# Kernel optimization log

Hardware: AMD Instinct MI355X
Metric: run time of the kernel (lower is better)

## Reference

```python
import jax, jax.numpy as jnp
import numpy as np

BINS = 128

def setup_inputs() -> dict:
    key = jax.random.key(0)
    k1, k2 = jax.random.split(key)
    B, S, F = 32, 16384, 64
    x = jax.random.uniform(k1, (B, S, F), dtype=jnp.float32)  # normalized to [0,1)
    weights = jnp.ones((BINS, F), dtype=jnp.float32)  # module inits weights to 1
    return {"input": x, "weights": weights}

def reference(input, weights):
    # input: [B, S, F]; weights: [bins, F]
    B, S, F = input.shape
    bins = weights.shape[0]
    # bin index per point per feature, truncation like torch .int()
    idx = jnp.clip((input * bins).astype(jnp.int32), 0, bins - 1)  # [B,S,F]
    # composite segment id: (b*F + f)*bins + bin  -> histogram without one-hot blowup
    b_idx = jnp.arange(B, dtype=jnp.int32)[:, None, None]
    f_idx = jnp.arange(F, dtype=jnp.int32)[None, None, :]
    seg = (b_idx * F + f_idx) * bins + idx  # [B,S,F]
    hist_flat = jax.ops.segment_sum(
        jnp.ones(seg.size, dtype=input.dtype),
        seg.reshape(-1),
        num_segments=B * F * bins,
    )
    hist = hist_flat.reshape(B, F, bins).transpose(0, 2, 1)  # [B, bins, F]
    return hist * weights[None, :, :]
```

## Files before the change

### kernel.cpp

```cpp
#include <hip/hip_runtime.h>

#define BINS 128
#define FEAT 64
#define SEG (BINS * FEAT)
#define B_DIM 32
#define S_DIM 16384
#define CHUNKS 16
#define THREADS 512
#define UNROLL 8

__global__ __launch_bounds__(THREADS, 2)
void hist_kernel(const float* __restrict__ x, unsigned* out) {
    __shared__ unsigned hist[SEG];
    for (int i = threadIdx.x; i < SEG; i += THREADS) hist[i] = 0u;
    __syncthreads();

    const int b    = blockIdx.y;
    const int lane = threadIdx.x & 63;
    const int wave = threadIdx.x >> 6;
    const int chunk = S_DIM / CHUNKS;
    const int rows_per_wave = chunk / (THREADS / 64);

    const float* xb = x + (long long)b * S_DIM * FEAT;
    const int s0 = blockIdx.x * chunk + wave * rows_per_wave;

    for (int it = 0; it < rows_per_wave; it += UNROLL) {
        float v[UNROLL];
        #pragma unroll
        for (int u = 0; u < UNROLL; ++u)
            v[u] = xb[(s0 + it + u) * FEAT + lane];
        #pragma unroll
        for (int u = 0; u < UNROLL; ++u) {
            int bin = (int)(v[u] * 128.0f);
            bin = bin < 0 ? 0 : (bin > 127 ? 127 : bin);
            atomicAdd(&hist[(bin << 6) + lane], 1u);
        }
    }
    __syncthreads();

    unsigned* gout = out + (size_t)b * SEG;
    for (int i = threadIdx.x; i < SEG; i += THREADS) {
        unsigned c = hist[i];
        if (c) atomicAdd(&gout[i], c);
    }
}

__global__ void finalize_kernel(const unsigned* cnt, float* out,
                                const float* __restrict__ w, int n) {
    int i = blockIdx.x * blockDim.x + threadIdx.x;
    if (i < n) {
        unsigned c = cnt[i];
        out[i] = (float)c * w[i & (SEG - 1)];
    }
}

extern "C" void kernel_launch(void* const* d_in, const int* in_sizes, int n_in,
                              void* d_out, int out_size, void* d_ws, size_t ws_size,
                              hipStream_t stream) {
    const float* x = (const float*)d_in[0];
    const float* w = (const float*)d_in[1];
    float* out = (float*)d_out;

    hipMemsetAsync(d_out, 0, (size_t)out_size * sizeof(float), stream);

    dim3 grid(CHUNKS, B_DIM);
    hist_kernel<<<grid, THREADS, 0, stream>>>(x, (unsigned*)d_out);

    int n = out_size;
    finalize_kernel<<<(n + 255) / 256, 256, 0, stream>>>((const unsigned*)d_out, out, w, n);
}
```

Before: 198.8 us.

## Replace global atomics with per-chunk partial histograms and vectorized reduction

Each block now writes its shared-memory histogram as a plain vectorized store into a per-chunk partial buffer in workspace. A finalize kernel sums the partials across chunks and applies the weights with uint4/float4 accesses. This removes the memset and the global atomic merge. The change also doubles the number of chunks and raises the launch-bounds occupancy hint for more parallelism. An atomic fallback is kept for when the workspace is too small. The cost is 16 MB of extra partial traffic, and whether the new path runs depends on the workspace size.

```diff
diff --git a/kernel.cpp b/kernel.cpp
--- a/kernel.cpp
+++ b/kernel.cpp
@@ -5,30 +5,93 @@
 #define SEG (BINS * FEAT)
 #define B_DIM 32
 #define S_DIM 16384
-#define CHUNKS 16
+#define CHUNKS 32
 #define THREADS 512
 #define UNROLL 8
+#define ROWS_PER_BLOCK (S_DIM / CHUNKS)
+#define ROWS_PER_WAVE  (ROWS_PER_BLOCK / (THREADS/64))
 
-__global__ __launch_bounds__(THREADS, 2)
-void hist_kernel(const float* __restrict__ x, unsigned* out) {
+
+__global__ __launch_bounds__(THREADS, 8)
+void hist_kernel(const float* __restrict__ x, unsigned* __restrict__ part) {
     __shared__ unsigned hist[SEG];
     for (int i = threadIdx.x; i < SEG; i += THREADS) hist[i] = 0u;
     __syncthreads();
 
+    const int c    = blockIdx.x;
     const int b    = blockIdx.y;
     const int lane = threadIdx.x & 63;
     const int wave = threadIdx.x >> 6;
-    const int chunk = S_DIM / CHUNKS;
-    const int rows_per_wave = chunk / (THREADS / 64);
 
-    const float* xb = x + (long long)b * S_DIM * FEAT;
-    const int s0 = blockIdx.x * chunk + wave * rows_per_wave;
+    const float* xb = x + ((size_t)b * S_DIM
+                           + (size_t)c * ROWS_PER_BLOCK
+                           + wave * ROWS_PER_WAVE) * FEAT;
 
-    for (int it = 0; it < rows_per_wave; it += UNROLL) {
+    for (int it = 0; it < ROWS_PER_WAVE; it += UNROLL) {
         float v[UNROLL];
         #pragma unroll
         for (int u = 0; u < UNROLL; ++u)
-            v[u] = xb[(s0 + it + u) * FEAT + lane];
+            v[u] = xb[(it + u) * FEAT + lane];
+        #pragma unroll
+        for (int u = 0; u < UNROLL; ++u) {
+            int bin = (int)(v[u] * 128.0f);
+            bin = bin < 0 ? 0 : (bin > 127 ? 127 : bin);
+            atomicAdd(&hist[(bin << 6) + lane], 1u);
+        }
+    }
+    __syncthreads();
+
+    unsigned* p = part + ((size_t)b * CHUNKS + c) * SEG;
+    for (int i = threadIdx.x * 4; i < SEG; i += THREADS * 4) {
+        uint4 v4 = *(const uint4*)&hist[i];
+        *(uint4*)&p[i] = v4;
+    }
+}
+
+__global__ __launch_bounds__(256)
+void finalize_kernel(const unsigned* __restrict__ part, float* __restrict__ out,
+                     const float* __restrict__ w) {
+    int t = blockIdx.x * blockDim.x + threadIdx.x;
+    int i = t * 4;
+    int b = i >> 13;
+    int j = i & (SEG - 1);
+
+    const unsigned* pb = part + (size_t)b * CHUNKS * SEG + j;
+    uint4 acc = make_uint4(0u, 0u, 0u, 0u);
+    for (int c = 0; c < CHUNKS; ++c) {
+        uint4 v = *(const uint4*)(pb + (size_t)c * SEG);
+        acc.x += v.x; acc.y += v.y; acc.z += v.z; acc.w += v.w;
+    }
+    float4 wv = *(const float4*)&w[j];
+    float4 o;
+    o.x = (float)acc.x * wv.x;
+    o.y = (float)acc.y * wv.y;
+    o.z = (float)acc.z * wv.z;
+    o.w = (float)acc.w * wv.w;
+    *(float4*)&out[i] = o;
+}
+
+
+__global__ __launch_bounds__(THREADS, 8)
+void hist_atomic_kernel(const float* __restrict__ x, unsigned* out) {
+    __shared__ unsigned hist[SEG];
+    for (int i = threadIdx.x; i < SEG; i += THREADS) hist[i] = 0u;
+    __syncthreads();
+
+    const int c    = blockIdx.x;
+    const int b    = blockIdx.y;
+    const int lane = threadIdx.x & 63;
+    const int wave = threadIdx.x >> 6;
+
+    const float* xb = x + ((size_t)b * S_DIM
+                           + (size_t)c * ROWS_PER_BLOCK
+                           + wave * ROWS_PER_WAVE) * FEAT;
+
+    for (int it = 0; it < ROWS_PER_WAVE; it += UNROLL) {
+        float v[UNROLL];
+        #pragma unroll
+        for (int u = 0; u < UNROLL; ++u)
+            v[u] = xb[(it + u) * FEAT + lane];
         #pragma unroll
         for (int u = 0; u < UNROLL; ++u) {
             int bin = (int)(v[u] * 128.0f);
@@ -40,17 +103,17 @@
 
     unsigned* gout = out + (size_t)b * SEG;
     for (int i = threadIdx.x; i < SEG; i += THREADS) {
-        unsigned c = hist[i];
-        if (c) atomicAdd(&gout[i], c);
+        unsigned cval = hist[i];
+        if (cval) atomicAdd(&gout[i], cval);
     }
 }
 
-__global__ void finalize_kernel(const unsigned* cnt, float* out,
-                                const float* __restrict__ w, int n) {
+__global__ void finalize_inplace_kernel(const unsigned* cnt, float* out,
+                                        const float* __restrict__ w, int n) {
     int i = blockIdx.x * blockDim.x + threadIdx.x;
     if (i < n) {
-        unsigned c = cnt[i];
-        out[i] = (float)c * w[i & (SEG - 1)];
+        unsigned cval = cnt[i];
+        out[i] = (float)cval * w[i & (SEG - 1)];
     }
 }
 
@@ -61,11 +124,19 @@
     const float* w = (const float*)d_in[1];
     float* out = (float*)d_out;
 
-    hipMemsetAsync(d_out, 0, (size_t)out_size * sizeof(float), stream);
+    const size_t part_bytes = (size_t)B_DIM * CHUNKS * SEG * sizeof(unsigned);
+    dim3 grid(CHUNKS, B_DIM);
 
-    dim3 grid(CHUNKS, B_DIM);
-    hist_kernel<<<grid, THREADS, 0, stream>>>(x, (unsigned*)d_out);
-
-    int n = out_size;
-    finalize_kernel<<<(n + 255) / 256, 256, 0, stream>>>((const unsigned*)d_out, out, w, n);
+    if (ws_size >= part_bytes && d_ws != nullptr) {
+        unsigned* part = (unsigned*)d_ws;
+        hist_kernel<<<grid, THREADS, 0, stream>>>(x, part);
+        int n_vec_threads = (B_DIM * SEG) / 4;
+        finalize_kernel<<<n_vec_threads / 256, 256, 0, stream>>>(part, out, w);
+    } else {
+        hipMemsetAsync(d_out, 0, (size_t)out_size * sizeof(float), stream);
+        hist_atomic_kernel<<<grid, THREADS, 0, stream>>>(x, (unsigned*)d_out);
+        int n = out_size;
+        finalize_inplace_kernel<<<(n + 255) / 256, 256, 0, stream>>>(
+            (const unsigned*)d_out, out, w, n);
+    }
 }
```

New measurement: 201.7 us. No clear change (+1.4%).
